# Kernel optimization log

Measured on AMD Instinct MI355X. Metric: run time of the kernel, lower is better.

## Reference

```python
import jax, jax.numpy as jnp
import numpy as np

THRESH_FACTOR = 0.7  # standard TTQ threshold: 0.7 * mean(|W|)

def ternary_quantize(w):
    delta = THRESH_FACTOR * jnp.mean(jnp.abs(w))
    # {-1, 0, +1} ternary weights
    return jnp.where(w > delta, 1.0, jnp.where(w < -delta, -1.0, 0.0)).astype(w.dtype)

def setup_inputs() -> dict:
    key = jax.random.key(0)
    k1, k2, k3 = jax.random.split(key, 3)
    B, S, D_IN, D_OUT = 8, 4096, 1024, 1024
    inp = {
        "input": jax.random.normal(k1, (B, S, D_IN), dtype=jnp.float32),
        "weight": jax.random.normal(k2, (D_OUT, D_IN), dtype=jnp.float32) * (1.0 / np.sqrt(D_IN)),
        "alpha": jnp.ones((1,), dtype=jnp.float32),
        "bias": jax.random.normal(k3, (D_OUT,), dtype=jnp.float32) * (1.0 / np.sqrt(D_IN)),
    }
    return inp

def reference(input, weight, alpha, bias):
    w_ternary = ternary_quantize(weight)          # [out, in] in {-1,0,1}
    w_eff = w_ternary * alpha                     # scalar alpha scale
    # F.linear: y = x @ W^T + b
    out = jnp.einsum('bsd,od->bso', input, w_eff) + bias
    return out
```

## Files before the change

### kernel.cpp

```cpp
#include <hip/hip_runtime.h>
#include <hip/hip_bf16.h>

typedef __bf16 bf16;
typedef __attribute__((ext_vector_type(8))) __bf16 bf16x8;
typedef __attribute__((ext_vector_type(4))) __bf16 bf16x4;
typedef __attribute__((ext_vector_type(4))) float f32x4;

#define BAR() __builtin_amdgcn_s_barrier()

__device__ __forceinline__ void async_load16(const void* g, void* l) {
    __builtin_amdgcn_global_load_lds(
        (const __attribute__((address_space(1))) void*)g,
        (__attribute__((address_space(3))) void*)l, 16, 0, 0);
}

__global__ __launch_bounds__(256) void k_abs_part(const float* __restrict__ w, int n,
                                                  double* __restrict__ part) {
    __shared__ double sd[256];
    const int per_block = n / gridDim.x;
    const int base = blockIdx.x * per_block;
    double s = 0.0;
    for (int i = threadIdx.x; i < per_block; i += 256)
        s += (double)fabsf(w[base + i]);
    sd[threadIdx.x] = s;
    __syncthreads();
    for (int off = 128; off > 0; off >>= 1) {
        if (threadIdx.x < off) sd[threadIdx.x] += sd[threadIdx.x + off];
        __syncthreads();
    }
    if (threadIdx.x == 0) part[blockIdx.x] = sd[0];
}

__global__ __launch_bounds__(256) void k_delta(const double* __restrict__ part, int npart,
                                               int n, float* __restrict__ delta) {
    __shared__ double sd[256];
    double s = 0.0;
    for (int i = threadIdx.x; i < npart; i += 256) s += part[i];
    sd[threadIdx.x] = s;
    __syncthreads();
    for (int off = 128; off > 0; off >>= 1) {
        if (threadIdx.x < off) sd[threadIdx.x] += sd[threadIdx.x + off];
        __syncthreads();
    }
    if (threadIdx.x == 0) *delta = (float)(0.7 * sd[0] / (double)n);
}

__global__ __launch_bounds__(256) void k_quant(const float* __restrict__ w,
                                               const float* __restrict__ dp,
                                               bf16* __restrict__ wt, int n4) {
    const float d = *dp;
    const int i = blockIdx.x * 256 + threadIdx.x;
    if (i >= n4) return;
    const float4 v = ((const float4*)w)[i];
    bf16x4 o;
    o[0] = (bf16)((v.x > d) ? 1.0f : (v.x < -d) ? -1.0f : 0.0f);
    o[1] = (bf16)((v.y > d) ? 1.0f : (v.y < -d) ? -1.0f : 0.0f);
    o[2] = (bf16)((v.z > d) ? 1.0f : (v.z < -d) ? -1.0f : 0.0f);
    o[3] = (bf16)((v.w > d) ? 1.0f : (v.w < -d) ? -1.0f : 0.0f);
    *(bf16x4*)(wt + (size_t)i * 4) = o;
}

__global__ __launch_bounds__(256) void k_convA(const float* __restrict__ x,
                                               bf16* __restrict__ y, int n8) {
    const int stride = gridDim.x * 256;
    for (int i = blockIdx.x * 256 + threadIdx.x; i < n8; i += stride) {
        const float4 a = ((const float4*)x)[2 * i];
        const float4 b = ((const float4*)x)[2 * i + 1];
        bf16x8 h;
        h[0] = (bf16)a.x; h[1] = (bf16)a.y; h[2] = (bf16)a.z; h[3] = (bf16)a.w;
        h[4] = (bf16)b.x; h[5] = (bf16)b.y; h[6] = (bf16)b.z; h[7] = (bf16)b.w;
        ((bf16x8*)y)[i] = h;
    }
}

__device__ __forceinline__ void stage_half(const bf16* __restrict__ srch, int K, int kt,
                                           char* dst, int t) {
    #pragma unroll
    for (int r = 0; r < 2; ++r) {
        const int c  = (r << 9) + t;
        const int rp = c >> 3;
        const int s  = (c & 7) ^ ((t >> 3) & 7);
        async_load16(srch + (size_t)rp * K + (kt << 6) + (s << 3), dst + (c << 4));
    }
}

__global__ __launch_bounds__(512, 2) void k_gemm8(const bf16* __restrict__ A,
                                                  const bf16* __restrict__ Bw,
                                                  const float* __restrict__ alphap,
                                                  const float* __restrict__ bias,
                                                  float* __restrict__ C,
                                                  int M, int N, int K) {
    __shared__ __align__(16) char lds[2][2][2][16384];

    const int t    = threadIdx.x;
    const int lane = t & 63;
    const int w    = t >> 6;
    const int wm   = w >> 2;
    const int wn   = w & 3;
    const int lr   = lane & 15;
    const int hi   = lane >> 4;

    const int nbn = N >> 8;
    const int cpx = gridDim.x >> 3;
    const int lid = (blockIdx.x & 7) * cpx + (blockIdx.x >> 3);
    const int bn0 = (lid % nbn) << 8;
    const int bm0 = (lid / nbn) << 8;

    const bf16* Asrc[2] = { A  + (size_t)bm0 * K,  A  + (size_t)(bm0 + 128) * K };
    const bf16* Bsrc[2] = { Bw + (size_t)bn0 * K,  Bw + (size_t)(bn0 + 128) * K };

    f32x4 acc[8][4] = {};
    bf16x8 afq[4][2], bfA[2][2], bfB[2][2];

    const int x0 = ((hi ^ (lr & 7)) << 4);
    const int x1 = (((4 + hi) ^ (lr & 7)) << 4);

#define LDA_Q(MQ, PAR) do { \
    const char* _b = &lds[PAR][0][wm][0]; \
    _Pragma("unroll") \
    for (int m = 0; m < 4; ++m) { \
        const int _r = ((MQ) << 6) + (m << 4) + lr; \
        afq[m][0] = *(const bf16x8*)(_b + _r * 128 + x0); \
        afq[m][1] = *(const bf16x8*)(_b + _r * 128 + x1); \
    } \
} while (0)

#define LDB_Q(DST, NQ, PAR) do { \
    const char* _b = &lds[PAR][1][wn >> 1][0]; \
    _Pragma("unroll") \
    for (int n = 0; n < 2; ++n) { \
        const int _r = ((wn & 1) << 6) + ((((NQ) << 1) + n) << 4) + lr; \
        DST[n][0] = *(const bf16x8*)(_b + _r * 128 + x0); \
        DST[n][1] = *(const bf16x8*)(_b + _r * 128 + x1); \
    } \
} while (0)

#define MF_Q(MQ, NQ, BF) do { \
    __builtin_amdgcn_s_setprio(1); \
    _Pragma("unroll") \
    for (int ks = 0; ks < 2; ++ks) \
        _Pragma("unroll") \
        for (int m = 0; m < 4; ++m) { \
            acc[((MQ)<<2)+m][((NQ)<<1)+0] = __builtin_amdgcn_mfma_f32_16x16x32_bf16(afq[m][ks], BF[0][ks], acc[((MQ)<<2)+m][((NQ)<<1)+0], 0, 0, 0); \
            acc[((MQ)<<2)+m][((NQ)<<1)+1] = __builtin_amdgcn_mfma_f32_16x16x32_bf16(afq[m][ks], BF[1][ks], acc[((MQ)<<2)+m][((NQ)<<1)+1], 0, 0, 0); \
        } \
    __builtin_amdgcn_s_setprio(0); \
} while (0)

#define VMCNT4() asm volatile("s_waitcnt vmcnt(4)" ::: "memory")

    stage_half(Bsrc[0], K, 0, &lds[0][1][0][0], t);
    stage_half(Bsrc[1], K, 0, &lds[0][1][1][0], t);
    stage_half(Asrc[0], K, 0, &lds[0][0][0][0], t);
    stage_half(Asrc[1], K, 0, &lds[0][0][1][0], t);
    stage_half(Bsrc[0], K, 1, &lds[1][1][0][0], t);
    stage_half(Bsrc[1], K, 1, &lds[1][1][1][0], t);
    asm volatile("s_waitcnt vmcnt(0)" ::: "memory");
    BAR();

    const int NI = K >> 7;
    for (int i = 0; i < NI; ++i) {
        const int  ktB  = 2 * i + 1;
        const bool last = (i == NI - 1);
        const int  kA2  = last ? 0 : 2 * i + 2;
        const int  kB2  = last ? 1 : 2 * i + 3;

        VMCNT4();
        LDA_Q(0, 0); LDB_Q(bfA, 0, 0);
        stage_half(Asrc[0], K, ktB, &lds[1][0][0][0], t);
        BAR(); MF_Q(0, 0, bfA); BAR();
        LDB_Q(bfB, 1, 0);
        stage_half(Asrc[1], K, ktB, &lds[1][0][1][0], t);
        BAR(); MF_Q(0, 1, bfB); BAR();
        LDA_Q(1, 0);
        stage_half(Bsrc[0], K, kA2, &lds[0][1][0][0], t);
        BAR(); MF_Q(1, 1, bfB); BAR();
        stage_half(Bsrc[1], K, kA2, &lds[0][1][1][0], t);
        BAR(); MF_Q(1, 0, bfA); BAR();

        VMCNT4();
        LDA_Q(0, 1); LDB_Q(bfA, 0, 1);
        stage_half(Asrc[0], K, kA2, &lds[0][0][0][0], t);
        BAR(); MF_Q(0, 0, bfA); BAR();
        LDB_Q(bfB, 1, 1);
        stage_half(Asrc[1], K, kA2, &lds[0][0][1][0], t);
        BAR(); MF_Q(0, 1, bfB); BAR();
        LDA_Q(1, 1);
        stage_half(Bsrc[0], K, kB2, &lds[1][1][0][0], t);
        BAR(); MF_Q(1, 1, bfB); BAR();
        stage_half(Bsrc[1], K, kB2, &lds[1][1][1][0], t);
        BAR(); MF_Q(1, 0, bfA); BAR();
    }

    const float alpha = *alphap;
    float bv[4];
    #pragma unroll
    for (int nf = 0; nf < 4; ++nf) bv[nf] = bias[bn0 + (wn << 6) + (nf << 4) + lr];

    #pragma unroll
    for (int mf = 0; mf < 8; ++mf) {
        const int grow = bm0 + (wm << 7) + (mf << 4) + (hi << 2);
        #pragma unroll
        for (int nf = 0; nf < 4; ++nf) {
            const int gcol = bn0 + (wn << 6) + (nf << 4) + lr;
            #pragma unroll
            for (int r = 0; r < 4; ++r)
                C[(size_t)(grow + r) * N + gcol] = alpha * acc[mf][nf][r] + bv[nf];
        }
    }
#undef LDA_Q
#undef LDB_Q
#undef MF_Q
#undef VMCNT4
}

__global__ __launch_bounds__(256) void k_gemm_fb(const float* __restrict__ A,
                                                 const bf16* __restrict__ Bw,
                                                 const float* __restrict__ alphap,
                                                 const float* __restrict__ bias,
                                                 float* __restrict__ C,
                                                 int M, int N, int K) {
    __shared__ bf16 As[128 * 32];
    __shared__ bf16 Bs[128 * 32];
    const int t = threadIdx.x, lane = t & 63, wave = t >> 6;
    const int nbm = M >> 7;
    const int bm0 = (blockIdx.x % nbm) << 7;
    const int bn0 = (blockIdx.x / nbm) << 7;
    const int wr = (wave >> 1) << 6, wc = (wave & 1) << 6;
    f32x4 acc[4][4] = {};
    const int lr = lane & 15, lk = (lane >> 4) << 3;
    for (int k0 = 0; k0 < K; k0 += 32) {
        #pragma unroll
        for (int j = 0; j < 2; ++j) {
            const int c = t + j * 256;
            async_load16(Bw + (size_t)(bn0 + (c >> 2)) * K + k0 + ((c & 3) << 3),
                         (char*)Bs + j * 4096 + wave * 1024);
        }
        #pragma unroll
        for (int i = 0; i < 4; ++i) {
            const int idx = t + i * 256;
            const int row = idx >> 3, c4 = (idx & 7) << 2;
            const float4 v = *(const float4*)(A + (size_t)(bm0 + row) * K + k0 + c4);
            bf16x4 h;
            h[0] = (bf16)v.x; h[1] = (bf16)v.y; h[2] = (bf16)v.z; h[3] = (bf16)v.w;
            *(bf16x4*)(As + row * 32 + c4) = h;
        }
        __syncthreads();
        bf16x8 af[4], bfr[4];
        #pragma unroll
        for (int m = 0; m < 4; ++m) af[m] = *(const bf16x8*)(As + (wr + m * 16 + lr) * 32 + lk);
        #pragma unroll
        for (int n = 0; n < 4; ++n) bfr[n] = *(const bf16x8*)(Bs + (wc + n * 16 + lr) * 32 + lk);
        #pragma unroll
        for (int m = 0; m < 4; ++m)
            #pragma unroll
            for (int n = 0; n < 4; ++n)
                acc[m][n] = __builtin_amdgcn_mfma_f32_16x16x32_bf16(af[m], bfr[n], acc[m][n], 0, 0, 0);
        __syncthreads();
    }
    const float alpha = *alphap;
    #pragma unroll
    for (int m = 0; m < 4; ++m)
        #pragma unroll
        for (int n = 0; n < 4; ++n) {
            const int gcol = bn0 + wc + n * 16 + lr;
            const float bv = bias[gcol];
            #pragma unroll
            for (int r = 0; r < 4; ++r) {
                const int grow = bm0 + wr + m * 16 + ((lane >> 4) << 2) + r;
                C[(size_t)grow * N + gcol] = alpha * acc[m][n][r] + bv;
            }
        }
}

extern "C" void kernel_launch(void* const* d_in, const int* in_sizes, int n_in,
                              void* d_out, int out_size, void* d_ws, size_t ws_size,
                              hipStream_t stream) {
    const float* x     = (const float*)d_in[0];
    const float* wgt   = (const float*)d_in[1];
    const float* alpha = (const float*)d_in[2];
    const float* bias  = (const float*)d_in[3];
    float* out = (float*)d_out;

    const int wn   = in_sizes[1];
    const int dout = in_sizes[3];
    const int din  = wn / dout;
    const int m    = in_sizes[0] / din;

    char* ws = (char*)d_ws;
    float*  delta = (float*)ws;
    double* part  = (double*)(ws + 64);
    bf16*   wt    = (bf16*)(ws + 8192);
    bf16*   abf   = (bf16*)(ws + (4u << 20));

    k_abs_part<<<256, 256, 0, stream>>>(wgt, wn, part);
    k_delta<<<1, 256, 0, stream>>>(part, 256, wn, delta);
    k_quant<<<(wn / 4 + 255) / 256, 256, 0, stream>>>(wgt, delta, wt, wn / 4);

    const size_t need = (4u << 20) + (size_t)in_sizes[0] * 2;
    if (ws_size >= need && (m % 256) == 0 && (dout % 256) == 0 && (din % 128) == 0) {
        k_convA<<<2048, 256, 0, stream>>>(x, abf, in_sizes[0] / 8);
        dim3 grid((m / 256) * (dout / 256));
        k_gemm8<<<grid, 512, 0, stream>>>(abf, wt, alpha, bias, out, m, dout, din);
    } else {
        dim3 grid((m / 128) * (dout / 128));
        k_gemm_fb<<<grid, 256, 0, stream>>>(x, wt, alpha, bias, out, m, dout, din);
    }
}
```

Measured before the change: 128.6 us.

## Fuse fp32-to-bf16 activation conversion into GEMM A-tile staging

Removes the separate activation conversion kernel and its bf16 workspace buffer. The GEMM now loads fp32 A tiles into registers, converts them to bf16 and writes them swizzled into LDS, while B keeps using async global-to-LDS loads. This removes a full write and reread of the activation, but A is now read as fp32 once per column tile, register pressure rises, and full vmcnt/lgkmcnt waits inside the loop reduce overlap.

```diff
diff --git a/kernel.cpp b/kernel.cpp
--- a/kernel.cpp
+++ b/kernel.cpp
@@ -60,19 +60,6 @@
     *(bf16x4*)(wt + (size_t)i * 4) = o;
 }
 
-__global__ __launch_bounds__(256) void k_convA(const float* __restrict__ x,
-                                               bf16* __restrict__ y, int n8) {
-    const int stride = gridDim.x * 256;
-    for (int i = blockIdx.x * 256 + threadIdx.x; i < n8; i += stride) {
-        const float4 a = ((const float4*)x)[2 * i];
-        const float4 b = ((const float4*)x)[2 * i + 1];
-        bf16x8 h;
-        h[0] = (bf16)a.x; h[1] = (bf16)a.y; h[2] = (bf16)a.z; h[3] = (bf16)a.w;
-        h[4] = (bf16)b.x; h[5] = (bf16)b.y; h[6] = (bf16)b.z; h[7] = (bf16)b.w;
-        ((bf16x8*)y)[i] = h;
-    }
-}
-
 __device__ __forceinline__ void stage_half(const bf16* __restrict__ srch, int K, int kt,
                                            char* dst, int t) {
     #pragma unroll
@@ -84,7 +71,7 @@
     }
 }
 
-__global__ __launch_bounds__(512, 2) void k_gemm8(const bf16* __restrict__ A,
+__global__ __launch_bounds__(512, 2) void k_gemm8(const float* __restrict__ Afp,
                                                   const bf16* __restrict__ Bw,
                                                   const float* __restrict__ alphap,
                                                   const float* __restrict__ bias,
@@ -106,14 +93,36 @@
     const int bn0 = (lid % nbn) << 8;
     const int bm0 = (lid / nbn) << 8;
 
-    const bf16* Asrc[2] = { A  + (size_t)bm0 * K,  A  + (size_t)(bm0 + 128) * K };
-    const bf16* Bsrc[2] = { Bw + (size_t)bn0 * K,  Bw + (size_t)(bn0 + 128) * K };
+    const bf16* Bsrc[2] = { Bw + (size_t)bn0 * K, Bw + (size_t)(bn0 + 128) * K };
 
     f32x4 acc[8][4] = {};
     bf16x8 afq[4][2], bfA[2][2], bfB[2][2];
+    float4 a0, a1, a2, a3;
+    float4 b0, b1, b2, b3;
 
     const int x0 = ((hi ^ (lr & 7)) << 4);
     const int x1 = (((4 + hi) ^ (lr & 7)) << 4);
+
+    const int a_r0 = t >> 3;
+    const int a_sl = t & 7;
+    const int a_sw = ((a_sl ^ (a_r0 & 7)) << 4);
+
+#define LA(H, KT, V0, V1, V2, V3) do { \
+    const float* _p = Afp + (size_t)(bm0 + ((H) << 7) + a_r0) * K + ((KT) << 6) + (a_sl << 3); \
+    V0 = *(const float4*)_p;                    V1 = *(const float4*)(_p + 4); \
+    V2 = *(const float4*)(_p + (size_t)64 * K); V3 = *(const float4*)(_p + (size_t)64 * K + 4); \
+} while (0)
+
+#define WA(PAR, H, V0, V1, V2, V3) do { \
+    char* _d = &lds[PAR][0][H][0]; \
+    bf16x8 _h0, _h1; \
+    _h0[0]=(bf16)V0.x; _h0[1]=(bf16)V0.y; _h0[2]=(bf16)V0.z; _h0[3]=(bf16)V0.w; \
+    _h0[4]=(bf16)V1.x; _h0[5]=(bf16)V1.y; _h0[6]=(bf16)V1.z; _h0[7]=(bf16)V1.w; \
+    _h1[0]=(bf16)V2.x; _h1[1]=(bf16)V2.y; _h1[2]=(bf16)V2.z; _h1[3]=(bf16)V2.w; \
+    _h1[4]=(bf16)V3.x; _h1[5]=(bf16)V3.y; _h1[6]=(bf16)V3.z; _h1[7]=(bf16)V3.w; \
+    *(bf16x8*)(_d + a_r0 * 128 + a_sw) = _h0; \
+    *(bf16x8*)(_d + (64 + a_r0) * 128 + a_sw) = _h1; \
+} while (0)
 
 #define LDA_Q(MQ, PAR) do { \
     const char* _b = &lds[PAR][0][wm][0]; \
@@ -147,15 +156,19 @@
     __builtin_amdgcn_s_setprio(0); \
 } while (0)
 
-#define VMCNT4() asm volatile("s_waitcnt vmcnt(4)" ::: "memory")
-
+#define VMCNT0() asm volatile("s_waitcnt vmcnt(0)" ::: "memory")
+#define LGKM0()  asm volatile("s_waitcnt lgkmcnt(0)" ::: "memory")
+
+    LA(0, 0, a0, a1, a2, a3);
+    LA(1, 0, b0, b1, b2, b3);
     stage_half(Bsrc[0], K, 0, &lds[0][1][0][0], t);
     stage_half(Bsrc[1], K, 0, &lds[0][1][1][0], t);
-    stage_half(Asrc[0], K, 0, &lds[0][0][0][0], t);
-    stage_half(Asrc[1], K, 0, &lds[0][0][1][0], t);
     stage_half(Bsrc[0], K, 1, &lds[1][1][0][0], t);
     stage_half(Bsrc[1], K, 1, &lds[1][1][1][0], t);
-    asm volatile("s_waitcnt vmcnt(0)" ::: "memory");
+    VMCNT0();
+    WA(0, 0, a0, a1, a2, a3);
+    WA(0, 1, b0, b1, b2, b3);
+    LGKM0();
     BAR();
 
     const int NI = K >> 7;
@@ -165,30 +178,35 @@
         const int  kA2  = last ? 0 : 2 * i + 2;
         const int  kB2  = last ? 1 : 2 * i + 3;
 
-        VMCNT4();
         LDA_Q(0, 0); LDB_Q(bfA, 0, 0);
-        stage_half(Asrc[0], K, ktB, &lds[1][0][0][0], t);
+        LA(0, ktB, a0, a1, a2, a3);
         BAR(); MF_Q(0, 0, bfA); BAR();
         LDB_Q(bfB, 1, 0);
-        stage_half(Asrc[1], K, ktB, &lds[1][0][1][0], t);
         BAR(); MF_Q(0, 1, bfB); BAR();
         LDA_Q(1, 0);
+        WA(1, 0, a0, a1, a2, a3);
         stage_half(Bsrc[0], K, kA2, &lds[0][1][0][0], t);
+        stage_half(Bsrc[1], K, kA2, &lds[0][1][1][0], t);
+        LA(1, ktB, b0, b1, b2, b3);
         BAR(); MF_Q(1, 1, bfB); BAR();
-        stage_half(Bsrc[1], K, kA2, &lds[0][1][1][0], t);
+        VMCNT0();
+        WA(1, 1, b0, b1, b2, b3);
+        LGKM0();
         BAR(); MF_Q(1, 0, bfA); BAR();
-
-        VMCNT4();
         LDA_Q(0, 1); LDB_Q(bfA, 0, 1);
-        stage_half(Asrc[0], K, kA2, &lds[0][0][0][0], t);
+        LA(0, kA2, a0, a1, a2, a3);
         BAR(); MF_Q(0, 0, bfA); BAR();
         LDB_Q(bfB, 1, 1);
-        stage_half(Asrc[1], K, kA2, &lds[0][0][1][0], t);
         BAR(); MF_Q(0, 1, bfB); BAR();
         LDA_Q(1, 1);
+        WA(0, 0, a0, a1, a2, a3);
         stage_half(Bsrc[0], K, kB2, &lds[1][1][0][0], t);
+        stage_half(Bsrc[1], K, kB2, &lds[1][1][1][0], t);
+        LA(1, kA2, b0, b1, b2, b3);
         BAR(); MF_Q(1, 1, bfB); BAR();
-        stage_half(Bsrc[1], K, kB2, &lds[1][1][1][0], t);
+        VMCNT0();
+        WA(0, 1, b0, b1, b2, b3);
+        LGKM0();
         BAR(); MF_Q(1, 0, bfA); BAR();
     }
 
@@ -208,10 +226,13 @@
                 C[(size_t)(grow + r) * N + gcol] = alpha * acc[mf][nf][r] + bv[nf];
         }
     }
+#undef LA
+#undef WA
 #undef LDA_Q
 #undef LDB_Q
 #undef MF_Q
-#undef VMCNT4
+#undef VMCNT0
+#undef LGKM0
 }
 
 __global__ __launch_bounds__(256) void k_gemm_fb(const float* __restrict__ A,
@@ -291,17 +312,14 @@
     float*  delta = (float*)ws;
     double* part  = (double*)(ws + 64);
     bf16*   wt    = (bf16*)(ws + 8192);
-    bf16*   abf   = (bf16*)(ws + (4u << 20));
 
     k_abs_part<<<256, 256, 0, stream>>>(wgt, wn, part);
     k_delta<<<1, 256, 0, stream>>>(part, 256, wn, delta);
     k_quant<<<(wn / 4 + 255) / 256, 256, 0, stream>>>(wgt, delta, wt, wn / 4);
 
-    const size_t need = (4u << 20) + (size_t)in_sizes[0] * 2;
-    if (ws_size >= need && (m % 256) == 0 && (dout % 256) == 0 && (din % 128) == 0) {
-        k_convA<<<2048, 256, 0, stream>>>(x, abf, in_sizes[0] / 8);
+    if ((m % 256) == 0 && (dout % 256) == 0 && (din % 128) == 0) {
         dim3 grid((m / 256) * (dout / 256));
-        k_gemm8<<<grid, 512, 0, stream>>>(abf, wt, alpha, bias, out, m, dout, din);
+        k_gemm8<<<grid, 512, 0, stream>>>(x, wt, alpha, bias, out, m, dout, din);
     } else {
         dim3 grid((m / 128) * (dout / 128));
         k_gemm_fb<<<grid, 256, 0, stream>>>(x, wt, alpha, bias, out, m, dout, din);
```

Result: slower. 161.0 us (+25.1%).
